# Optimization experiments

Hardware: AMD Instinct MI355X
Metric: run time of the kernel (lower is better)

## Reference

```python
import jax, jax.numpy as jnp
import numpy as np

K = 7          # window kernel size
PAD = 3        # padding so out spatial == in spatial (stride=1, dilation=1)
BN_EPS = 1e-5


def conv1x1(x, w, b):
    # x: (b,c,h,w), w: (o,c), b: (o,)
    return jnp.einsum('bchw,oc->bohw', x, w) + b[None, :, None, None]


def bn_relu(x, bn):
    # bn: (4, C) rows = gamma, beta, running_mean, running_var (inference-mode BN)
    g, bta, m, v = bn[0], bn[1], bn[2], bn[3]
    scale = g / jnp.sqrt(v + BN_EPS)
    y = (x - m[None, :, None, None]) * scale[None, :, None, None] + bta[None, :, None, None]
    return jax.nn.relu(y)


def extract_patches(x):
    # Equivalent of F.unfold(x, K, padding=PAD, stride=1) reshaped to (b, C, K*K, H, W).
    # Ordering matches torch: channel major, kernel positions row-major.
    b, c, h, w = x.shape
    xp = jnp.pad(x, ((0, 0), (0, 0), (PAD, PAD), (PAD, PAD)))
    ps = [xp[:, :, i:i + h, j:j + w] for i in range(K) for j in range(K)]
    return jnp.stack(ps, axis=2)  # (b, c, K*K, h, w)


def setup_inputs() -> dict:
    key = jax.random.key(0)
    ks = jax.random.split(key, 20)
    Cin, Ck, Cv, Co = 256, 64, 128, 256
    b, h, w = 2, 96, 96

    def wgt(k, o, c):
        return jax.random.normal(k, (o, c), jnp.float32) * 0.05

    def bias(k, o):
        return jax.random.normal(k, (o,), jnp.float32) * 0.02

    def bn(k, c):
        g = 1.0 + 0.1 * jax.random.normal(k, (c,), jnp.float32)
        bta = 0.1 * jax.random.normal(jax.random.fold_in(k, 1), (c,), jnp.float32)
        m = 0.05 * jax.random.normal(jax.random.fold_in(k, 2), (c,), jnp.float32)
        v = 1.0 + 0.1 * jax.random.uniform(jax.random.fold_in(k, 3), (c,), jnp.float32)
        return jnp.stack([g, bta, m, v])  # (4, c)

    return {
        'x': jax.random.normal(ks[0], (b, Cin, h, w), jnp.float32),
        'fk_w1': wgt(ks[1], Ck, Cin), 'fk_b1': bias(ks[2], Ck), 'fk_bn1': bn(ks[3], Ck),
        'fk_w2': wgt(ks[4], Ck, Ck), 'fk_b2': bias(ks[5], Ck), 'fk_bn2': bn(ks[6], Ck),
        'fq_w1': wgt(ks[7], Ck, Cin), 'fq_b1': bias(ks[8], Ck), 'fq_bn1': bn(ks[9], Ck),
        'fq_w2': wgt(ks[10], Ck, Ck), 'fq_b2': bias(ks[11], Ck), 'fq_bn2': bn(ks[12], Ck),
        'fv_w': wgt(ks[13], Cv, Cin), 'fv_b': bias(ks[14], Cv),
        'W_w': wgt(ks[15], Co, Cv), 'W_b': bias(ks[16], Co),
    }


def reference(x, fk_w1, fk_b1, fk_bn1, fk_w2, fk_b2, fk_bn2,
              fq_w1, fq_b1, fq_bn1, fq_w2, fq_b2, fq_bn2,
              fv_w, fv_b, W_w, W_b):
    # scale=1 -> no pooling. stride=1, dilation=1, pad=3, k=7 -> out spatial == in spatial.
    value = conv1x1(x, fv_w, fv_b)                       # (b, Cv, H, W)
    unfold_value = extract_patches(value)                # (b, Cv, 49, H, W)

    k1 = bn_relu(conv1x1(x, fk_w1, fk_b1), fk_bn1)
    key = bn_relu(conv1x1(k1, fk_w2, fk_b2), fk_bn2)     # (b, Ck, H, W)
    unfold_key = extract_patches(key)                    # (b, Ck, 49, H, W)

    q1 = bn_relu(conv1x1(x, fq_w1, fq_b1), fq_bn1)
    query = bn_relu(conv1x1(q1, fq_w2, fq_b2), fq_bn2)   # (b, Ck, H, W)
    # start_index = dilation*(k//2) - padding = 0; stride=1 -> query slice is identity.

    sim = jnp.sum(unfold_key * query[:, :, None], axis=1, keepdims=True)  # (b,1,49,H,W)
    sim = jax.nn.softmax(sim, axis=2)
    context = jnp.sum(sim * unfold_value, axis=2)        # (b, Cv, H, W)
    context = conv1x1(context, W_w, W_b)                 # (b, Co, H, W)
    # F.interpolate to (h, w) with align_corners=True is identity (same size).
    return context
```

## Files before the change

kernel.cpp:

```cpp
#include <hip/hip_runtime.h>
#include <hip/hip_bf16.h>

typedef _Float16 f16;
typedef _Float16 f16x4 __attribute__((ext_vector_type(4)));
typedef _Float16 f16x8 __attribute__((ext_vector_type(8)));
typedef float f32x4 __attribute__((ext_vector_type(4)));

#define HH 96
#define WW 96
#define HWs 9216
#define BN_EPS 1e-5f

#define OFF_ACT1 0u
#define OFF_ACT2 4718592u
#define OFF_W1   9437184u
#define OFF_W2   9568256u
#define OFF_W3   9584640u
#define OFF_ST   9650176u

__global__ __launch_bounds__(256) void prep_kernel(
    const float* __restrict__ fk_w1, const float* __restrict__ fk_b1, const float* __restrict__ fk_bn1,
    const float* __restrict__ fk_w2, const float* __restrict__ fk_b2, const float* __restrict__ fk_bn2,
    const float* __restrict__ fq_w1, const float* __restrict__ fq_b1, const float* __restrict__ fq_bn1,
    const float* __restrict__ fq_w2, const float* __restrict__ fq_b2, const float* __restrict__ fq_bn2,
    const float* __restrict__ fv_w,  const float* __restrict__ fv_b,
    const float* __restrict__ W_w,   const float* __restrict__ W_b,
    char* __restrict__ wsb)
{
  f16* w1 = (f16*)(wsb + OFF_W1);
  f16* w2 = (f16*)(wsb + OFF_W2);
  f16* w3 = (f16*)(wsb + OFF_W3);
  float* st = (float*)(wsb + OFF_ST);
  int i = blockIdx.x * 256 + threadIdx.x;
  if (i < 65536) {
    int o = i >> 8, c = i & 255;
    float v;
    if (o < 128)      v = fv_w[o * 256 + c];
    else if (o < 192) v = fk_w1[(o - 128) * 256 + c];
    else              v = fq_w1[(o - 192) * 256 + c];
    w1[i] = (f16)v;
  } else if (i < 73728) {
    int j = i - 65536; int o = j >> 6, c = j & 63;
    w2[j] = (f16)((o < 64) ? fk_w2[o * 64 + c] : fq_w2[(o - 64) * 64 + c]);
  } else if (i < 106496) {
    int j = i - 73728;
    w3[j] = (f16)W_w[j];
  } else if (i < 106752) {
    int o = i - 106496;
    float s, t;
    if (o < 128) { s = 1.0f; t = fv_b[o]; }
    else if (o < 192) {
      int j = o - 128;
      float g = fk_bn1[j], be = fk_bn1[64 + j], m = fk_bn1[128 + j], v = fk_bn1[192 + j];
      s = g * rsqrtf(v + BN_EPS); t = (fk_b1[j] - m) * s + be;
    } else {
      int j = o - 192;
      float g = fq_bn1[j], be = fq_bn1[64 + j], m = fq_bn1[128 + j], v = fq_bn1[192 + j];
      s = g * rsqrtf(v + BN_EPS); t = (fq_b1[j] - m) * s + be;
    }
    st[o] = s; st[256 + o] = t;
  } else if (i < 106880) {
    int o = i - 106752;
    float s, t;
    if (o < 64) {
      float g = fk_bn2[o], be = fk_bn2[64 + o], m = fk_bn2[128 + o], v = fk_bn2[192 + o];
      s = g * rsqrtf(v + BN_EPS); t = (fk_b2[o] - m) * s + be;
    } else {
      int j = o - 64;
      float g = fq_bn2[j], be = fq_bn2[64 + j], m = fq_bn2[128 + j], v = fq_bn2[192 + j];
      s = g * rsqrtf(v + BN_EPS); t = (fq_b2[j] - m) * s + be;
    }
    st[512 + o] = s; st[640 + o] = t;
  } else if (i < 107136) {
    int o = i - 106880;
    st[768 + o] = W_b[o];
  }
}

__global__ __launch_bounds__(256) void conv12(
    const float* __restrict__ x, const f16* __restrict__ W1, const f16* __restrict__ W2,
    f16* __restrict__ act1, f16* __restrict__ act2, const float* __restrict__ st)
{
  __shared__ f16 As[32 * 40];
  __shared__ f16 Bs[256 * 40];
  __shared__ f16 kqs[2][32 * 72];
  const int tid = threadIdx.x;
  const int l = tid & 63, w = tid >> 6;
  const int bb = blockIdx.y;
  const int p0 = blockIdx.x * 32;
  const int lrow = l & 15, lk = (l >> 4) * 8;

  f32x4 acc[2][4];
#pragma unroll
  for (int i = 0; i < 2; i++)
#pragma unroll
    for (int j = 0; j < 4; j++) acc[i][j] = (f32x4){0.f, 0.f, 0.f, 0.f};

  const int spx = tid & 31, skg = tid >> 5;
#pragma unroll 1
  for (int ks = 0; ks < 8; ks++) {
    f16x4 av;
#pragma unroll
    for (int j = 0; j < 4; j++)
      av[j] = (f16)x[((size_t)bb * 256 + ks * 32 + skg * 4 + j) * HWs + p0 + spx];
    *(f16x4*)&As[spx * 40 + skg * 4] = av;
#pragma unroll
    for (int it = 0; it < 4; it++) {
      int tt = it * 256 + tid;
      int row = tt >> 2, seg = tt & 3;
      *(f16x8*)&Bs[row * 40 + seg * 8] =
          *(const f16x8*)&W1[(size_t)row * 256 + ks * 32 + seg * 8];
    }
    __syncthreads();
    f16x8 a[2], b[4];
#pragma unroll
    for (int mi = 0; mi < 2; mi++) a[mi] = *(const f16x8*)&As[(mi * 16 + lrow) * 40 + lk];
#pragma unroll
    for (int nj = 0; nj < 4; nj++) b[nj] = *(const f16x8*)&Bs[(w * 64 + nj * 16 + lrow) * 40 + lk];
#pragma unroll
    for (int mi = 0; mi < 2; mi++)
#pragma unroll
      for (int nj = 0; nj < 4; nj++)
        acc[mi][nj] = __builtin_amdgcn_mfma_f32_16x16x32_f16(a[mi], b[nj], acc[mi][nj], 0, 0, 0);
    __syncthreads();
  }

#pragma unroll
  for (int mi = 0; mi < 2; mi++)
#pragma unroll
    for (int nj = 0; nj < 4; nj++) {
      int cout = w * 64 + nj * 16 + lrow;
      float s = st[cout], t = st[256 + cout];
#pragma unroll
      for (int r = 0; r < 4; r++) {
        int px = mi * 16 + (l >> 4) * 4 + r;
        float v = acc[mi][nj][r] * s + t;
        if (w < 2) {
          act1[((size_t)bb * HWs + p0 + px) * 128 + cout] = (f16)v;
        } else {
          kqs[w - 2][px * 72 + (nj * 16 + lrow)] = (f16)fmaxf(v, 0.f);
        }
      }
    }
  __syncthreads();

  const int sel = w >> 1, half = w & 1;
  const f16* W2s = W2 + sel * 64 * 64;
  f32x4 acc2[2][2];
#pragma unroll
  for (int i = 0; i < 2; i++)
#pragma unroll
    for (int j = 0; j < 2; j++) acc2[i][j] = (f32x4){0.f, 0.f, 0.f, 0.f};
#pragma unroll
  for (int ks = 0; ks < 2; ks++) {
    f16x8 a2[2], b2[2];
#pragma unroll
    for (int mi = 0; mi < 2; mi++)
      a2[mi] = *(const f16x8*)&kqs[sel][(mi * 16 + lrow) * 72 + ks * 32 + lk];
#pragma unroll
    for (int nj = 0; nj < 2; nj++)
      b2[nj] = *(const f16x8*)&W2s[(size_t)(half * 32 + nj * 16 + lrow) * 64 + ks * 32 + lk];
#pragma unroll
    for (int mi = 0; mi < 2; mi++)
#pragma unroll
      for (int nj = 0; nj < 2; nj++)
        acc2[mi][nj] = __builtin_amdgcn_mfma_f32_16x16x32_f16(a2[mi], b2[nj], acc2[mi][nj], 0, 0, 0);
  }
#pragma unroll
  for (int mi = 0; mi < 2; mi++)
#pragma unroll
    for (int nj = 0; nj < 2; nj++) {
      int c2 = sel * 64 + half * 32 + nj * 16 + lrow;
      float s = st[512 + c2], t = st[640 + c2];
#pragma unroll
      for (int r = 0; r < 4; r++) {
        int px = mi * 16 + (l >> 4) * 4 + r;
        float v = fmaxf(acc2[mi][nj][r] * s + t, 0.f);
        act2[((size_t)bb * HWs + p0 + px) * 128 + c2] = (f16)v;
      }
    }
}

__global__ __launch_bounds__(256) void attn_final(const f16* __restrict__ act1,
                                                  const f16* __restrict__ act2,
                                                  const f16* __restrict__ W3,
                                                  const float* __restrict__ st,
                                                  float* __restrict__ out)
{
  __shared__ float Ps[64 * 52];
  __shared__ f16 buf[208 * 136];
  const int tid = threadIdx.x;
  const int l = tid & 63, w = tid >> 6;
  const int bb = blockIdx.z;
  const int x0 = blockIdx.x * 8, y0 = blockIdx.y * 8;
  const f16* a2 = act2 + (size_t)bb * HWs * 128;
  const f16* a1 = act1 + (size_t)bb * HWs * 128;
  f16* Qs = buf;
  f16* Ks = buf + 64 * 72;
  const int lrow = l & 15, lk = (l >> 4) * 8;

#pragma unroll
  for (int it = 0; it < 2; it++) {
    int t = it * 256 + tid;
    int q = t >> 3, seg = t & 7;
    int gp = (y0 + (q >> 3)) * WW + x0 + (q & 7);
    *(f16x8*)&Qs[q * 72 + seg * 8] = *(const f16x8*)&a2[(size_t)gp * 128 + 64 + seg * 8];
  }
  for (int t = tid; t < 1664; t += 256) {
    int kk = t >> 3, seg = t & 7;
    int ky = (kk * 4682) >> 16, kx = kk - 14 * ky;
    int gy = y0 - 3 + ky, gx = x0 - 3 + kx;
    f16x8 v = {(f16)0, (f16)0, (f16)0, (f16)0, (f16)0, (f16)0, (f16)0, (f16)0};
    if (kk < 196 && (unsigned)gy < (unsigned)HH && (unsigned)gx < (unsigned)WW)
      v = *(const f16x8*)&a2[((size_t)(gy * WW + gx)) * 128 + seg * 8];
    *(f16x8*)&Ks[kk * 72 + seg * 8] = v;
  }
  __syncthreads();

  f32x4 sc[13];
#pragma unroll
  for (int nj = 0; nj < 13; nj++) sc[nj] = (f32x4){0.f, 0.f, 0.f, 0.f};
#pragma unroll
  for (int ks = 0; ks < 2; ks++) {
    f16x8 aq = *(const f16x8*)&Qs[(w * 16 + lrow) * 72 + ks * 32 + lk];
#pragma unroll
    for (int nj = 0; nj < 13; nj++) {
      f16x8 bk = *(const f16x8*)&Ks[(nj * 16 + lrow) * 72 + ks * 32 + lk];
      sc[nj] = __builtin_amdgcn_mfma_f32_16x16x32_f16(aq, bk, sc[nj], 0, 0, 0);
    }
  }
  const int r0 = w * 16 + (l >> 4) * 4;
#pragma unroll
  for (int nj = 0; nj < 13; nj++) {
    int c = nj * 16 + lrow;
    int ky = (c * 4682) >> 16, kx = c - 14 * ky;
#pragma unroll
    for (int r = 0; r < 4; r++) {
      int qy = (r0 + r) >> 3, qx = (r0 + r) & 7;
      bool valid = ((unsigned)(ky - qy) < 7u) && ((unsigned)(kx - qx) < 7u);
      if (!valid) sc[nj][r] = -1e30f;
    }
  }
  float mx[4], sm[4], inv[4];
#pragma unroll
  for (int r = 0; r < 4; r++) {
    mx[r] = -1e30f;
#pragma unroll
    for (int nj = 0; nj < 13; nj++) mx[r] = fmaxf(mx[r], sc[nj][r]);
  }
#pragma unroll
  for (int off = 1; off < 16; off <<= 1)
#pragma unroll
    for (int r = 0; r < 4; r++) mx[r] = fmaxf(mx[r], __shfl_xor(mx[r], off));
#pragma unroll
  for (int r = 0; r < 4; r++) sm[r] = 0.f;
#pragma unroll
  for (int nj = 0; nj < 13; nj++)
#pragma unroll
    for (int r = 0; r < 4; r++) {
      float e = __expf(sc[nj][r] - mx[r]);
      sc[nj][r] = e; sm[r] += e;
    }
#pragma unroll
  for (int off = 1; off < 16; off <<= 1)
#pragma unroll
    for (int r = 0; r < 4; r++) sm[r] += __shfl_xor(sm[r], off);
#pragma unroll
  for (int r = 0; r < 4; r++) inv[r] = 1.0f / sm[r];
#pragma unroll
  for (int nj = 0; nj < 13; nj++) {
    int c = nj * 16 + lrow;
    int ky = (c * 4682) >> 16, kx = c - 14 * ky;
#pragma unroll
    for (int r = 0; r < 4; r++) {
      int qy = (r0 + r) >> 3, qx = (r0 + r) & 7;
      int dy = ky - qy, dx = kx - qx;
      if (((unsigned)dy < 7u) && ((unsigned)dx < 7u))
        Ps[(r0 + r) * 52 + dy * 7 + dx] = sc[nj][r] * inv[r];
    }
  }
  __syncthreads();

  f16* Vs = buf;
  for (int t = tid; t < 3328; t += 256) {
    int kk = t >> 4, seg = t & 15;
    int ky = (kk * 4682) >> 16, kx = kk - 14 * ky;
    int gy = y0 - 3 + ky, gx = x0 - 3 + kx;
    f16x8 v = {(f16)0, (f16)0, (f16)0, (f16)0, (f16)0, (f16)0, (f16)0, (f16)0};
    if (kk < 196 && (unsigned)gy < (unsigned)HH && (unsigned)gx < (unsigned)WW)
      v = *(const f16x8*)&a1[((size_t)(gy * WW + gx)) * 128 + seg * 8];
    *(f16x8*)&Vs[kk * 136 + seg * 8] = v;
  }
  __syncthreads();

  const int q = tid >> 2;
  const int qy = q >> 3, qx = q & 7;
  const int ch0 = (tid & 3) * 32;
  float acc[32];
#pragma unroll
  for (int i = 0; i < 32; i++) acc[i] = 0.f;
#pragma unroll
  for (int dy = 0; dy < 7; dy++)
#pragma unroll
    for (int dx = 0; dx < 7; dx++) {
      float p = Ps[q * 52 + dy * 7 + dx];
      int kk = (qy + dy) * 14 + qx + dx;
      const f16* vp = &Vs[kk * 136 + ch0];
#pragma unroll
      for (int s = 0; s < 4; s++) {
        f16x8 v = *(const f16x8*)&vp[s * 8];
#pragma unroll
        for (int j = 0; j < 8; j++) acc[s * 8 + j] += (float)v[j] * p;
      }
    }
  __syncthreads();

  f16* ctxs = buf;
#pragma unroll
  for (int s = 0; s < 4; s++) {
    f16x8 o;
#pragma unroll
    for (int j = 0; j < 8; j++) o[j] = (f16)acc[s * 8 + j];
    *(f16x8*)&ctxs[q * 136 + ch0 + s * 8] = o;
  }
  __syncthreads();

  f32x4 fac[4][4];
#pragma unroll
  for (int i = 0; i < 4; i++)
#pragma unroll
    for (int j = 0; j < 4; j++) fac[i][j] = (f32x4){0.f, 0.f, 0.f, 0.f};
#pragma unroll
  for (int ks = 0; ks < 4; ks++) {
    f16x8 a3[4], b3[4];
#pragma unroll
    for (int mi = 0; mi < 4; mi++)
      a3[mi] = *(const f16x8*)&W3[(size_t)(w * 64 + mi * 16 + lrow) * 128 + ks * 32 + lk];
#pragma unroll
    for (int nj = 0; nj < 4; nj++)
      b3[nj] = *(const f16x8*)&ctxs[(nj * 16 + lrow) * 136 + ks * 32 + lk];
#pragma unroll
    for (int mi = 0; mi < 4; mi++)
#pragma unroll
      for (int nj = 0; nj < 4; nj++)
        fac[mi][nj] = __builtin_amdgcn_mfma_f32_16x16x32_f16(a3[mi], b3[nj], fac[mi][nj], 0, 0, 0);
  }
#pragma unroll
  for (int mi = 0; mi < 4; mi++)
#pragma unroll
    for (int nj = 0; nj < 4; nj++) {
#pragma unroll
      for (int r = 0; r < 4; r++) {
        int cout = w * 64 + mi * 16 + (l >> 4) * 4 + r;
        int px = nj * 16 + lrow;
        int gp = (y0 + (px >> 3)) * WW + x0 + (px & 7);
        out[((size_t)bb * 256 + cout) * HWs + gp] = fac[mi][nj][r] + st[768 + cout];
      }
    }
}

extern "C" void kernel_launch(void* const* d_in, const int* in_sizes, int n_in,
                              void* d_out, int out_size, void* d_ws, size_t ws_size,
                              hipStream_t stream) {
  (void)in_sizes; (void)n_in; (void)out_size; (void)ws_size;
  const float* x      = (const float*)d_in[0];
  const float* fk_w1  = (const float*)d_in[1];
  const float* fk_b1  = (const float*)d_in[2];
  const float* fk_bn1 = (const float*)d_in[3];
  const float* fk_w2  = (const float*)d_in[4];
  const float* fk_b2  = (const float*)d_in[5];
  const float* fk_bn2 = (const float*)d_in[6];
  const float* fq_w1  = (const float*)d_in[7];
  const float* fq_b1  = (const float*)d_in[8];
  const float* fq_bn1 = (const float*)d_in[9];
  const float* fq_w2  = (const float*)d_in[10];
  const float* fq_b2  = (const float*)d_in[11];
  const float* fq_bn2 = (const float*)d_in[12];
  const float* fv_w   = (const float*)d_in[13];
  const float* fv_b   = (const float*)d_in[14];
  const float* W_w    = (const float*)d_in[15];
  const float* W_b    = (const float*)d_in[16];
  char* wsb = (char*)d_ws;
  float* out = (float*)d_out;

  f16* act1 = (f16*)(wsb + OFF_ACT1);
  f16* act2 = (f16*)(wsb + OFF_ACT2);
  f16* w1   = (f16*)(wsb + OFF_W1);
  f16* w2   = (f16*)(wsb + OFF_W2);
  f16* w3   = (f16*)(wsb + OFF_W3);
  float* st = (float*)(wsb + OFF_ST);

  prep_kernel<<<dim3(419), dim3(256), 0, stream>>>(
      fk_w1, fk_b1, fk_bn1, fk_w2, fk_b2, fk_bn2,
      fq_w1, fq_b1, fq_bn1, fq_w2, fq_b2, fq_bn2, fv_w, fv_b, W_w, W_b, wsb);

  conv12<<<dim3(288, 2), dim3(256), 0, stream>>>(x, w1, w2, act1, act2, st);

  attn_final<<<dim3(12, 12, 2), dim3(256), 0, stream>>>(act1, act2, w3, st, out);
}
```

Baseline: 138.9 us.

## Drop prep kernel and halve attention tile height to double grid

Removes the separate weight-conversion and BN-folding kernel: conv12 and attn_final now read fp32 weights directly, convert them to fp16 on the fly, and compute BN scale and shift inline. This saves a kernel launch and a workspace round trip, at the cost of redundant conversion work in every block. The attention kernel also shrinks its tile from 8x8 to 4x8 queries, doubling the grid from 288 to 576 blocks to improve occupancy and CU coverage. In exchange, only two of four waves compute scores, and the key/value halo overhead per query grows.

```diff
diff --git a/kernel.cpp b/kernel.cpp
--- a/kernel.cpp
+++ b/kernel.cpp
@@ -13,73 +13,17 @@
 
 #define OFF_ACT1 0u
 #define OFF_ACT2 4718592u
-#define OFF_W1   9437184u
-#define OFF_W2   9568256u
-#define OFF_W3   9584640u
-#define OFF_ST   9650176u
-
-__global__ __launch_bounds__(256) void prep_kernel(
-    const float* __restrict__ fk_w1, const float* __restrict__ fk_b1, const float* __restrict__ fk_bn1,
-    const float* __restrict__ fk_w2, const float* __restrict__ fk_b2, const float* __restrict__ fk_bn2,
-    const float* __restrict__ fq_w1, const float* __restrict__ fq_b1, const float* __restrict__ fq_bn1,
-    const float* __restrict__ fq_w2, const float* __restrict__ fq_b2, const float* __restrict__ fq_bn2,
-    const float* __restrict__ fv_w,  const float* __restrict__ fv_b,
-    const float* __restrict__ W_w,   const float* __restrict__ W_b,
-    char* __restrict__ wsb)
-{
-  f16* w1 = (f16*)(wsb + OFF_W1);
-  f16* w2 = (f16*)(wsb + OFF_W2);
-  f16* w3 = (f16*)(wsb + OFF_W3);
-  float* st = (float*)(wsb + OFF_ST);
-  int i = blockIdx.x * 256 + threadIdx.x;
-  if (i < 65536) {
-    int o = i >> 8, c = i & 255;
-    float v;
-    if (o < 128)      v = fv_w[o * 256 + c];
-    else if (o < 192) v = fk_w1[(o - 128) * 256 + c];
-    else              v = fq_w1[(o - 192) * 256 + c];
-    w1[i] = (f16)v;
-  } else if (i < 73728) {
-    int j = i - 65536; int o = j >> 6, c = j & 63;
-    w2[j] = (f16)((o < 64) ? fk_w2[o * 64 + c] : fq_w2[(o - 64) * 64 + c]);
-  } else if (i < 106496) {
-    int j = i - 73728;
-    w3[j] = (f16)W_w[j];
-  } else if (i < 106752) {
-    int o = i - 106496;
-    float s, t;
-    if (o < 128) { s = 1.0f; t = fv_b[o]; }
-    else if (o < 192) {
-      int j = o - 128;
-      float g = fk_bn1[j], be = fk_bn1[64 + j], m = fk_bn1[128 + j], v = fk_bn1[192 + j];
-      s = g * rsqrtf(v + BN_EPS); t = (fk_b1[j] - m) * s + be;
-    } else {
-      int j = o - 192;
-      float g = fq_bn1[j], be = fq_bn1[64 + j], m = fq_bn1[128 + j], v = fq_bn1[192 + j];
-      s = g * rsqrtf(v + BN_EPS); t = (fq_b1[j] - m) * s + be;
-    }
-    st[o] = s; st[256 + o] = t;
-  } else if (i < 106880) {
-    int o = i - 106752;
-    float s, t;
-    if (o < 64) {
-      float g = fk_bn2[o], be = fk_bn2[64 + o], m = fk_bn2[128 + o], v = fk_bn2[192 + o];
-      s = g * rsqrtf(v + BN_EPS); t = (fk_b2[o] - m) * s + be;
-    } else {
-      int j = o - 64;
-      float g = fq_bn2[j], be = fq_bn2[64 + j], m = fq_bn2[128 + j], v = fq_bn2[192 + j];
-      s = g * rsqrtf(v + BN_EPS); t = (fq_b2[j] - m) * s + be;
-    }
-    st[512 + o] = s; st[640 + o] = t;
-  } else if (i < 107136) {
-    int o = i - 106880;
-    st[768 + o] = W_b[o];
-  }
-}
 
 __global__ __launch_bounds__(256) void conv12(
-    const float* __restrict__ x, const f16* __restrict__ W1, const f16* __restrict__ W2,
-    f16* __restrict__ act1, f16* __restrict__ act2, const float* __restrict__ st)
+    const float* __restrict__ x,
+    const float* __restrict__ fv_w, const float* __restrict__ fk_w1, const float* __restrict__ fq_w1,
+    const float* __restrict__ fk_w2, const float* __restrict__ fq_w2,
+    const float* __restrict__ fv_b,
+    const float* __restrict__ fk_b1, const float* __restrict__ fk_bn1,
+    const float* __restrict__ fq_b1, const float* __restrict__ fq_bn1,
+    const float* __restrict__ fk_b2, const float* __restrict__ fk_bn2,
+    const float* __restrict__ fq_b2, const float* __restrict__ fq_bn2,
+    f16* __restrict__ act1, f16* __restrict__ act2)
 {
   __shared__ f16 As[32 * 40];
   __shared__ f16 Bs[256 * 40];
@@ -108,8 +52,15 @@
     for (int it = 0; it < 4; it++) {
       int tt = it * 256 + tid;
       int row = tt >> 2, seg = tt & 3;
-      *(f16x8*)&Bs[row * 40 + seg * 8] =
-          *(const f16x8*)&W1[(size_t)row * 256 + ks * 32 + seg * 8];
+      const float* srcp;
+      if (it < 2)      srcp = fv_w  + (size_t)row * 256;
+      else if (it == 2) srcp = fk_w1 + (size_t)(row - 128) * 256;
+      else              srcp = fq_w1 + (size_t)(row - 192) * 256;
+      float4 u0 = *(const float4*)&srcp[ks * 32 + seg * 8];
+      float4 u1 = *(const float4*)&srcp[ks * 32 + seg * 8 + 4];
+      f16x8 h = {(f16)u0.x, (f16)u0.y, (f16)u0.z, (f16)u0.w,
+                 (f16)u1.x, (f16)u1.y, (f16)u1.z, (f16)u1.w};
+      *(f16x8*)&Bs[row * 40 + seg * 8] = h;
     }
     __syncthreads();
     f16x8 a[2], b[4];
@@ -126,11 +77,19 @@
   }
 
 #pragma unroll
-  for (int mi = 0; mi < 2; mi++)
-#pragma unroll
-    for (int nj = 0; nj < 4; nj++) {
-      int cout = w * 64 + nj * 16 + lrow;
-      float s = st[cout], t = st[256 + cout];
+  for (int nj = 0; nj < 4; nj++) {
+    int cout = w * 64 + nj * 16 + lrow;
+    float s, t;
+    if (w < 2) { s = 1.0f; t = fv_b[cout]; }
+    else {
+      int j = nj * 16 + lrow;
+      const float* bn = (w == 2) ? fk_bn1 : fq_bn1;
+      const float* bs = (w == 2) ? fk_b1 : fq_b1;
+      float g = bn[j], be = bn[64 + j], m = bn[128 + j], v = bn[192 + j];
+      s = g * rsqrtf(v + BN_EPS); t = (bs[j] - m) * s + be;
+    }
+#pragma unroll
+    for (int mi = 0; mi < 2; mi++)
 #pragma unroll
       for (int r = 0; r < 4; r++) {
         int px = mi * 16 + (l >> 4) * 4 + r;
@@ -141,11 +100,11 @@
           kqs[w - 2][px * 72 + (nj * 16 + lrow)] = (f16)fmaxf(v, 0.f);
         }
       }
-    }
+  }
   __syncthreads();
 
   const int sel = w >> 1, half = w & 1;
-  const f16* W2s = W2 + sel * 64 * 64;
+  const float* W2s = sel ? fq_w2 : fk_w2;
   f32x4 acc2[2][2];
 #pragma unroll
   for (int i = 0; i < 2; i++)
@@ -158,8 +117,13 @@
     for (int mi = 0; mi < 2; mi++)
       a2[mi] = *(const f16x8*)&kqs[sel][(mi * 16 + lrow) * 72 + ks * 32 + lk];
 #pragma unroll
-    for (int nj = 0; nj < 2; nj++)
-      b2[nj] = *(const f16x8*)&W2s[(size_t)(half * 32 + nj * 16 + lrow) * 64 + ks * 32 + lk];
+    for (int nj = 0; nj < 2; nj++) {
+      const float* wp = &W2s[(size_t)(half * 32 + nj * 16 + lrow) * 64 + ks * 32 + lk];
+      float4 u0 = *(const float4*)&wp[0];
+      float4 u1 = *(const float4*)&wp[4];
+      b2[nj] = (f16x8){(f16)u0.x, (f16)u0.y, (f16)u0.z, (f16)u0.w,
+                       (f16)u1.x, (f16)u1.y, (f16)u1.z, (f16)u1.w};
+    }
 #pragma unroll
     for (int mi = 0; mi < 2; mi++)
 #pragma unroll
@@ -167,138 +131,141 @@
         acc2[mi][nj] = __builtin_amdgcn_mfma_f32_16x16x32_f16(a2[mi], b2[nj], acc2[mi][nj], 0, 0, 0);
   }
 #pragma unroll
-  for (int mi = 0; mi < 2; mi++)
-#pragma unroll
-    for (int nj = 0; nj < 2; nj++) {
-      int c2 = sel * 64 + half * 32 + nj * 16 + lrow;
-      float s = st[512 + c2], t = st[640 + c2];
+  for (int nj = 0; nj < 2; nj++) {
+    int j2 = half * 32 + nj * 16 + lrow;
+    int c2 = sel * 64 + j2;
+    const float* bn = sel ? fq_bn2 : fk_bn2;
+    const float* bs = sel ? fq_b2 : fk_b2;
+    float g = bn[j2], be = bn[64 + j2], m = bn[128 + j2], v = bn[192 + j2];
+    float s = g * rsqrtf(v + BN_EPS), t = (bs[j2] - m) * s + be;
+#pragma unroll
+    for (int mi = 0; mi < 2; mi++)
 #pragma unroll
       for (int r = 0; r < 4; r++) {
         int px = mi * 16 + (l >> 4) * 4 + r;
-        float v = fmaxf(acc2[mi][nj][r] * s + t, 0.f);
-        act2[((size_t)bb * HWs + p0 + px) * 128 + c2] = (f16)v;
-      }
-    }
+        float vv = fmaxf(acc2[mi][nj][r] * s + t, 0.f);
+        act2[((size_t)bb * HWs + p0 + px) * 128 + c2] = (f16)vv;
+      }
+  }
 }
 
 __global__ __launch_bounds__(256) void attn_final(const f16* __restrict__ act1,
                                                   const f16* __restrict__ act2,
-                                                  const f16* __restrict__ W3,
-                                                  const float* __restrict__ st,
+                                                  const float* __restrict__ W_w,
+                                                  const float* __restrict__ W_b,
                                                   float* __restrict__ out)
 {
-  __shared__ float Ps[64 * 52];
-  __shared__ f16 buf[208 * 136];
+  __shared__ f16 Qs[32 * 72];
+  __shared__ f16 Ks[144 * 72];
+  __shared__ f16 Vs[144 * 136];
+  __shared__ float Ps[32 * 52];
   const int tid = threadIdx.x;
   const int l = tid & 63, w = tid >> 6;
   const int bb = blockIdx.z;
-  const int x0 = blockIdx.x * 8, y0 = blockIdx.y * 8;
+  const int x0 = blockIdx.x * 8, y0 = blockIdx.y * 4;
   const f16* a2 = act2 + (size_t)bb * HWs * 128;
   const f16* a1 = act1 + (size_t)bb * HWs * 128;
-  f16* Qs = buf;
-  f16* Ks = buf + 64 * 72;
   const int lrow = l & 15, lk = (l >> 4) * 8;
 
-#pragma unroll
-  for (int it = 0; it < 2; it++) {
-    int t = it * 256 + tid;
-    int q = t >> 3, seg = t & 7;
+  {
+    int q = tid >> 3, seg = tid & 7;
     int gp = (y0 + (q >> 3)) * WW + x0 + (q & 7);
     *(f16x8*)&Qs[q * 72 + seg * 8] = *(const f16x8*)&a2[(size_t)gp * 128 + 64 + seg * 8];
   }
-  for (int t = tid; t < 1664; t += 256) {
+  for (int t = tid; t < 1152; t += 256) {
     int kk = t >> 3, seg = t & 7;
     int ky = (kk * 4682) >> 16, kx = kk - 14 * ky;
     int gy = y0 - 3 + ky, gx = x0 - 3 + kx;
     f16x8 v = {(f16)0, (f16)0, (f16)0, (f16)0, (f16)0, (f16)0, (f16)0, (f16)0};
-    if (kk < 196 && (unsigned)gy < (unsigned)HH && (unsigned)gx < (unsigned)WW)
+    if (kk < 140 && (unsigned)gy < (unsigned)HH && (unsigned)gx < (unsigned)WW)
       v = *(const f16x8*)&a2[((size_t)(gy * WW + gx)) * 128 + seg * 8];
     *(f16x8*)&Ks[kk * 72 + seg * 8] = v;
   }
-  __syncthreads();
-
-  f32x4 sc[13];
-#pragma unroll
-  for (int nj = 0; nj < 13; nj++) sc[nj] = (f32x4){0.f, 0.f, 0.f, 0.f};
-#pragma unroll
-  for (int ks = 0; ks < 2; ks++) {
-    f16x8 aq = *(const f16x8*)&Qs[(w * 16 + lrow) * 72 + ks * 32 + lk];
-#pragma unroll
-    for (int nj = 0; nj < 13; nj++) {
-      f16x8 bk = *(const f16x8*)&Ks[(nj * 16 + lrow) * 72 + ks * 32 + lk];
-      sc[nj] = __builtin_amdgcn_mfma_f32_16x16x32_f16(aq, bk, sc[nj], 0, 0, 0);
-    }
-  }
-  const int r0 = w * 16 + (l >> 4) * 4;
-#pragma unroll
-  for (int nj = 0; nj < 13; nj++) {
-    int c = nj * 16 + lrow;
-    int ky = (c * 4682) >> 16, kx = c - 14 * ky;
-#pragma unroll
-    for (int r = 0; r < 4; r++) {
-      int qy = (r0 + r) >> 3, qx = (r0 + r) & 7;
-      bool valid = ((unsigned)(ky - qy) < 7u) && ((unsigned)(kx - qx) < 7u);
-      if (!valid) sc[nj][r] = -1e30f;
-    }
-  }
-  float mx[4], sm[4], inv[4];
-#pragma unroll
-  for (int r = 0; r < 4; r++) {
-    mx[r] = -1e30f;
-#pragma unroll
-    for (int nj = 0; nj < 13; nj++) mx[r] = fmaxf(mx[r], sc[nj][r]);
-  }
-#pragma unroll
-  for (int off = 1; off < 16; off <<= 1)
-#pragma unroll
-    for (int r = 0; r < 4; r++) mx[r] = fmaxf(mx[r], __shfl_xor(mx[r], off));
-#pragma unroll
-  for (int r = 0; r < 4; r++) sm[r] = 0.f;
-#pragma unroll
-  for (int nj = 0; nj < 13; nj++)
-#pragma unroll
-    for (int r = 0; r < 4; r++) {
-      float e = __expf(sc[nj][r] - mx[r]);
-      sc[nj][r] = e; sm[r] += e;
-    }
-#pragma unroll
-  for (int off = 1; off < 16; off <<= 1)
-#pragma unroll
-    for (int r = 0; r < 4; r++) sm[r] += __shfl_xor(sm[r], off);
-#pragma unroll
-  for (int r = 0; r < 4; r++) inv[r] = 1.0f / sm[r];
-#pragma unroll
-  for (int nj = 0; nj < 13; nj++) {
-    int c = nj * 16 + lrow;
-    int ky = (c * 4682) >> 16, kx = c - 14 * ky;
-#pragma unroll
-    for (int r = 0; r < 4; r++) {
-      int qy = (r0 + r) >> 3, qx = (r0 + r) & 7;
-      int dy = ky - qy, dx = kx - qx;
-      if (((unsigned)dy < 7u) && ((unsigned)dx < 7u))
-        Ps[(r0 + r) * 52 + dy * 7 + dx] = sc[nj][r] * inv[r];
-    }
-  }
-  __syncthreads();
-
-  f16* Vs = buf;
-  for (int t = tid; t < 3328; t += 256) {
+  for (int t = tid; t < 2304; t += 256) {
     int kk = t >> 4, seg = t & 15;
     int ky = (kk * 4682) >> 16, kx = kk - 14 * ky;
     int gy = y0 - 3 + ky, gx = x0 - 3 + kx;
     f16x8 v = {(f16)0, (f16)0, (f16)0, (f16)0, (f16)0, (f16)0, (f16)0, (f16)0};
-    if (kk < 196 && (unsigned)gy < (unsigned)HH && (unsigned)gx < (unsigned)WW)
+    if (kk < 140 && (unsigned)gy < (unsigned)HH && (unsigned)gx < (unsigned)WW)
       v = *(const f16x8*)&a1[((size_t)(gy * WW + gx)) * 128 + seg * 8];
     *(f16x8*)&Vs[kk * 136 + seg * 8] = v;
   }
   __syncthreads();
 
-  const int q = tid >> 2;
+  if (w < 2) {
+    f32x4 sc[9];
+#pragma unroll
+    for (int nj = 0; nj < 9; nj++) sc[nj] = (f32x4){0.f, 0.f, 0.f, 0.f};
+#pragma unroll
+    for (int ks = 0; ks < 2; ks++) {
+      f16x8 aq = *(const f16x8*)&Qs[(w * 16 + lrow) * 72 + ks * 32 + lk];
+#pragma unroll
+      for (int nj = 0; nj < 9; nj++) {
+        f16x8 bk = *(const f16x8*)&Ks[(nj * 16 + lrow) * 72 + ks * 32 + lk];
+        sc[nj] = __builtin_amdgcn_mfma_f32_16x16x32_f16(aq, bk, sc[nj], 0, 0, 0);
+      }
+    }
+    const int r0 = w * 16 + (l >> 4) * 4;
+#pragma unroll
+    for (int nj = 0; nj < 9; nj++) {
+      int c = nj * 16 + lrow;
+      int ky = (c * 4682) >> 16, kx = c - 14 * ky;
+#pragma unroll
+      for (int r = 0; r < 4; r++) {
+        int row = r0 + r;
+        int qy = (row >> 3), qx = row & 7;
+        bool valid = (c < 140) && ((unsigned)(ky - qy) < 7u) && ((unsigned)(kx - qx) < 7u);
+        if (!valid) sc[nj][r] = -1e30f;
+      }
+    }
+    float mx[4], sm[4], inv[4];
+#pragma unroll
+    for (int r = 0; r < 4; r++) {
+      mx[r] = -1e30f;
+#pragma unroll
+      for (int nj = 0; nj < 9; nj++) mx[r] = fmaxf(mx[r], sc[nj][r]);
+    }
+#pragma unroll
+    for (int off = 1; off < 16; off <<= 1)
+#pragma unroll
+      for (int r = 0; r < 4; r++) mx[r] = fmaxf(mx[r], __shfl_xor(mx[r], off));
+#pragma unroll
+    for (int r = 0; r < 4; r++) sm[r] = 0.f;
+#pragma unroll
+    for (int nj = 0; nj < 9; nj++)
+#pragma unroll
+      for (int r = 0; r < 4; r++) {
+        float e = __expf(sc[nj][r] - mx[r]);
+        sc[nj][r] = e; sm[r] += e;
+      }
+#pragma unroll
+    for (int off = 1; off < 16; off <<= 1)
+#pragma unroll
+      for (int r = 0; r < 4; r++) sm[r] += __shfl_xor(sm[r], off);
+#pragma unroll
+    for (int r = 0; r < 4; r++) inv[r] = 1.0f / sm[r];
+#pragma unroll
+    for (int nj = 0; nj < 9; nj++) {
+      int c = nj * 16 + lrow;
+      int ky = (c * 4682) >> 16, kx = c - 14 * ky;
+#pragma unroll
+      for (int r = 0; r < 4; r++) {
+        int row = r0 + r;
+        int qy = (row >> 3), qx = row & 7;
+        int dy = ky - qy, dx = kx - qx;
+        if (c < 140 && ((unsigned)dy < 7u) && ((unsigned)dx < 7u))
+          Ps[row * 52 + dy * 7 + dx] = sc[nj][r] * inv[r];
+      }
+    }
+  }
+  __syncthreads();
+
+  const int q = tid >> 3, c8 = tid & 7;
   const int qy = q >> 3, qx = q & 7;
-  const int ch0 = (tid & 3) * 32;
-  float acc[32];
-#pragma unroll
-  for (int i = 0; i < 32; i++) acc[i] = 0.f;
+  const int ch0 = c8 * 16;
+  float acc[16];
+#pragma unroll
+  for (int i = 0; i < 16; i++) acc[i] = 0.f;
 #pragma unroll
   for (int dy = 0; dy < 7; dy++)
 #pragma unroll
@@ -306,55 +273,61 @@
       float p = Ps[q * 52 + dy * 7 + dx];
       int kk = (qy + dy) * 14 + qx + dx;
       const f16* vp = &Vs[kk * 136 + ch0];
-#pragma unroll
-      for (int s = 0; s < 4; s++) {
-        f16x8 v = *(const f16x8*)&vp[s * 8];
-#pragma unroll
-        for (int j = 0; j < 8; j++) acc[s * 8 + j] += (float)v[j] * p;
-      }
-    }
-  __syncthreads();
-
-  f16* ctxs = buf;
-#pragma unroll
-  for (int s = 0; s < 4; s++) {
-    f16x8 o;
-#pragma unroll
-    for (int j = 0; j < 8; j++) o[j] = (f16)acc[s * 8 + j];
-    *(f16x8*)&ctxs[q * 136 + ch0 + s * 8] = o;
-  }
-  __syncthreads();
-
-  f32x4 fac[4][4];
+      f16x8 v0 = *(const f16x8*)&vp[0];
+      f16x8 v1 = *(const f16x8*)&vp[8];
+#pragma unroll
+      for (int j = 0; j < 8; j++) {
+        acc[j] += (float)v0[j] * p;
+        acc[8 + j] += (float)v1[j] * p;
+      }
+    }
+  __syncthreads();
+
+  {
+    f16x8 o0, o1;
+#pragma unroll
+    for (int j = 0; j < 8; j++) { o0[j] = (f16)acc[j]; o1[j] = (f16)acc[8 + j]; }
+    *(f16x8*)&Vs[q * 136 + ch0] = o0;
+    *(f16x8*)&Vs[q * 136 + ch0 + 8] = o1;
+  }
+  __syncthreads();
+
+  f32x4 fac[4][2];
 #pragma unroll
   for (int i = 0; i < 4; i++)
 #pragma unroll
-    for (int j = 0; j < 4; j++) fac[i][j] = (f32x4){0.f, 0.f, 0.f, 0.f};
+    for (int j = 0; j < 2; j++) fac[i][j] = (f32x4){0.f, 0.f, 0.f, 0.f};
 #pragma unroll
   for (int ks = 0; ks < 4; ks++) {
-    f16x8 a3[4], b3[4];
+    f16x8 a3[4], b3[2];
+#pragma unroll
+    for (int mi = 0; mi < 4; mi++) {
+      const float* wp = &W_w[(size_t)(w * 64 + mi * 16 + lrow) * 128 + ks * 32 + lk];
+      float4 u0 = *(const float4*)&wp[0];
+      float4 u1 = *(const float4*)&wp[4];
+      a3[mi] = (f16x8){(f16)u0.x, (f16)u0.y, (f16)u0.z, (f16)u0.w,
+                       (f16)u1.x, (f16)u1.y, (f16)u1.z, (f16)u1.w};
+    }
+#pragma unroll
+    for (int nj = 0; nj < 2; nj++)
+      b3[nj] = *(const f16x8*)&Vs[(nj * 16 + lrow) * 136 + ks * 32 + lk];
 #pragma unroll
     for (int mi = 0; mi < 4; mi++)
-      a3[mi] = *(const f16x8*)&W3[(size_t)(w * 64 + mi * 16 + lrow) * 128 + ks * 32 + lk];
-#pragma unroll
-    for (int nj = 0; nj < 4; nj++)
-      b3[nj] = *(const f16x8*)&ctxs[(nj * 16 + lrow) * 136 + ks * 32 + lk];
-#pragma unroll
-    for (int mi = 0; mi < 4; mi++)
-#pragma unroll
-      for (int nj = 0; nj < 4; nj++)
+#pragma unroll
+      for (int nj = 0; nj < 2; nj++)
         fac[mi][nj] = __builtin_amdgcn_mfma_f32_16x16x32_f16(a3[mi], b3[nj], fac[mi][nj], 0, 0, 0);
   }
 #pragma unroll
   for (int mi = 0; mi < 4; mi++)
 #pragma unroll
-    for (int nj = 0; nj < 4; nj++) {
-#pragma unroll
-      for (int r = 0; r < 4; r++) {
-        int cout = w * 64 + mi * 16 + (l >> 4) * 4 + r;
+    for (int r = 0; r < 4; r++) {
+      int cout = w * 64 + mi * 16 + (l >> 4) * 4 + r;
+      float bias = W_b[cout];
+#pragma unroll
+      for (int nj = 0; nj < 2; nj++) {
         int px = nj * 16 + lrow;
         int gp = (y0 + (px >> 3)) * WW + x0 + (px & 7);
-        out[((size_t)bb * 256 + cout) * HWs + gp] = fac[mi][nj][r] + st[768 + cout];
+        out[((size_t)bb * 256 + cout) * HWs + gp] = fac[mi][nj][r] + bias;
       }
     }
 }
@@ -385,16 +358,11 @@
 
   f16* act1 = (f16*)(wsb + OFF_ACT1);
   f16* act2 = (f16*)(wsb + OFF_ACT2);
-  f16* w1   = (f16*)(wsb + OFF_W1);
-  f16* w2   = (f16*)(wsb + OFF_W2);
-  f16* w3   = (f16*)(wsb + OFF_W3);
-  float* st = (float*)(wsb + OFF_ST);
-
-  prep_kernel<<<dim3(419), dim3(256), 0, stream>>>(
-      fk_w1, fk_b1, fk_bn1, fk_w2, fk_b2, fk_bn2,
-      fq_w1, fq_b1, fq_bn1, fq_w2, fq_b2, fq_bn2, fv_w, fv_b, W_w, W_b, wsb);
-
-  conv12<<<dim3(288, 2), dim3(256), 0, stream>>>(x, w1, w2, act1, act2, st);
-
-  attn_final<<<dim3(12, 12, 2), dim3(256), 0, stream>>>(act1, act2, w3, st, out);
+
+  conv12<<<dim3(288, 2), dim3(256), 0, stream>>>(
+      x, fv_w, fk_w1, fq_w1, fk_w2, fq_w2,
+      fv_b, fk_b1, fk_bn1, fq_b1, fq_bn1,
+      fk_b2, fk_bn2, fq_b2, fq_bn2, act1, act2);
+
+  attn_final<<<dim3(12, 24, 2), dim3(256), 0, stream>>>(act1, act2, W_w, W_b, out);
 }
```

After: 156.8 us. 12.9% more time.
